# Optimization experiments

Measured on AMD Instinct MI355X. Metric: run time of the kernel, lower is better.

Reference implementation:

```python
import jax, jax.numpy as jnp
import numpy as np

# Module constants (from init_kwargs)
NUM_PREFIX = 8
NUM_LAYERS = 32
NUM_SUB = NUM_LAYERS - NUM_PREFIX  # 24
H = 32            # attention heads
RANK = 2          # scheduler_rank: heads are gated in groups of RANK
TAU = 5.0
HIDDEN = 4096
B = 16384


def setup_inputs() -> dict:
    key = jax.random.key(0)
    k1, k2, k3, k4 = jax.random.split(key, 4)
    x = jax.random.normal(k1, (B, HIDDEN), dtype=jnp.float32)
    latency = jax.random.uniform(k2, (B,), dtype=jnp.float32)
    W = jax.random.normal(k3, (HIDDEN, NUM_SUB * H * 2), dtype=jnp.float32) * 0.02
    b = jnp.zeros((NUM_SUB * H * 2,), dtype=jnp.float32)
    u = jax.random.uniform(k4, (B, NUM_SUB, H, 2), dtype=jnp.float32)
    return {"x": x, "latency": latency, "W": W, "b": b, "u": u}


def reference(x, latency, W, b, u):
    min_units = NUM_PREFIX * H // RANK   # 128
    max_units = NUM_LAYERS * H // RANK   # 512
    # latency_quantizing: snap continuous latency to integer head-group budget
    units = jnp.clip(jnp.round(latency * max_units), min_units, max_units)
    budget = units - min_units           # (B,) groups to activate in sub layers

    logits = (x @ W + b).reshape(B, NUM_SUB, H, 2)  # 2-way keep/drop per head

    # Gumbel-softmax (soft probs) from pre-sampled uniform noise
    eps = 1e-6
    g = -jnp.log(-jnp.log(u * (1.0 - 2.0 * eps) + eps))
    soft = jax.nn.softmax((logits + g) / TAU, axis=-1)  # (B, L, H, 2)
    p_keep = soft[..., 0]                               # (B, L, H)

    # Group heads by RANK, score groups, keep the top-`budget` groups per sample
    G = H // RANK
    scores = p_keep.reshape(B, NUM_SUB * G, RANK).mean(-1)   # (B, 384)
    ranks = jnp.argsort(jnp.argsort(-scores, axis=-1), axis=-1)
    hard_group = (ranks < budget[:, None]).astype(x.dtype)   # (B, 384)
    hard_keep = jnp.repeat(hard_group, RANK, axis=-1).reshape(B, NUM_SUB, H)
    hard = jnp.stack([hard_keep, 1.0 - hard_keep], axis=-1)  # (B, L, H, 2)

    # Straight-through hard sample
    out = hard + soft - jax.lax.stop_gradient(soft)          # (B, L, H, 2)
    out = jnp.moveaxis(out, -1, 2)                           # (B, L, 2, H)

    prefix = jnp.ones((B, NUM_PREFIX, 2, H), dtype=out.dtype)
    return jnp.concatenate([prefix, out], axis=1)            # (B, 32, 2, H)
```

## Files before the change

### kernel.cpp

```cpp
#include <hip/hip_runtime.h>
#include <math.h>

#define BATCH  16384
#define HID    4096
#define NCOLS  1536
#define NGRP   384

#define GAP_MIN 2.0e-5f
#define MARG    1.0e-5f
#define WMAX    16

typedef unsigned short u16;
typedef short bf16x8 __attribute__((ext_vector_type(8)));
typedef float f32x4  __attribute__((ext_vector_type(4)));

__device__ __forceinline__ int budget_of(float lat) {
    float un = rintf(lat * 512.0f);
    un = fminf(fmaxf(un, 128.0f), 512.0f);
    return (int)un - 128;
}

__device__ __forceinline__ double gumbel_d(float uu) {
    double v = (double)uu * (1.0 - 2.0e-6) + 1.0e-6;
    return -log(-log(v));
}

__device__ __forceinline__ float gumbel_f(float u) {
    float inner;
    if (u <= 0.5f) {
        float v = fmaf(u, 0.999998f, 1e-6f);
        inner = -logf(v);
    } else {
        float t1 = 1.0f - u;
        float w  = fmaf(1e-6f, fmaf(2.0f, u, -1.0f), t1);
        inner = -log1pf(-w);
    }
    return -logf(inner);
}

__device__ __forceinline__ float score_f(float l0, float l1, float l2, float l3,
                                         float4 uv) {
    const float d0 = ((l0 + gumbel_f(uv.x)) - (l1 + gumbel_f(uv.y))) * 0.2f;
    const float d1 = ((l2 + gumbel_f(uv.z)) - (l3 + gumbel_f(uv.w))) * 0.2f;
    const float p0 = 1.0f / (1.0f + expf(-d0));
    const float p1 = 1.0f / (1.0f + expf(-d1));
    return 0.5f * (p0 + p1);
}

__device__ __forceinline__ unsigned bf16_rne_bits(float f) {
    unsigned b = __float_as_uint(f);
    return (b + 0x7FFFu + ((b >> 16) & 1u)) >> 16;
}

__device__ __forceinline__ void split4(const float4 v, uint2& hi, uint2& lo) {
    const unsigned bx = __float_as_uint(v.x), by = __float_as_uint(v.y),
                   bz = __float_as_uint(v.z), bw = __float_as_uint(v.w);
    const unsigned hx = bx & 0xFFFF0000u, hy = by & 0xFFFF0000u,
                   hz = bz & 0xFFFF0000u, hw = bw & 0xFFFF0000u;
    hi.x = (hx >> 16) | hy;
    hi.y = (hz >> 16) | hw;
    const float lx = v.x - __uint_as_float(hx);
    const float ly = v.y - __uint_as_float(hy);
    const float lz = v.z - __uint_as_float(hz);
    const float lw = v.w - __uint_as_float(hw);
    lo.x = bf16_rne_bits(lx) | (bf16_rne_bits(ly) << 16);
    lo.y = bf16_rne_bits(lz) | (bf16_rne_bits(lw) << 16);
}

__device__ __forceinline__ void gload16(const u16* g, u16* l) {
    __builtin_amdgcn_global_load_lds(
        (const __attribute__((address_space(1))) unsigned int*)g,
        (__attribute__((address_space(3))) unsigned int*)l, 16, 0, 0);
}

__global__ __launch_bounds__(64)
void prefilter_kernel(const float* __restrict__ latency, float* __restrict__ out)
{
    const int b = blockIdx.x;
    const int t = threadIdx.x;
    const int budget = budget_of(latency[b]);
    float* obase = out + (size_t)b * 2048;

    const float4 ones = make_float4(1.f, 1.f, 1.f, 1.f);
    ((float4*)obase)[t]      = ones;
    ((float4*)obase)[t + 64] = ones;

    if (!(budget > 0 && budget < NGRP)) {
        const float K = (budget == 0) ? 0.0f : 1.0f;
#pragma unroll
        for (int j = 0; j < 6; ++j) {
            const int i = j * 64 + t;
            const int p = i * 4;
            const int s = (p >> 5) & 1;
            const float v = s ? (1.0f - K) : K;
            ((float4*)(obase + 512))[i] = make_float4(v, v, v, v);
        }
    }
}

__global__ __launch_bounds__(256)
void idx_build(const float* __restrict__ latency, int* __restrict__ count,
               int* __restrict__ idx)
{
    const int s = blockIdx.x * 256 + threadIdx.x;
    const int budget = budget_of(latency[s]);
    const bool interior = (budget > 0 && budget < NGRP);
    const unsigned long long m = __ballot(interior);
    const int lane = threadIdx.x & 63;
    int base = 0;
    if (lane == 0 && m) base = atomicAdd(count, __popcll(m));
    base = __shfl(base, 0);
    if (interior)
        idx[base + __popcll(m & ((1ull << lane) - 1ull))] = s;
}

__global__ __launch_bounds__(256)
void convert_w(const float* __restrict__ W, u16* __restrict__ wt_hi,
               u16* __restrict__ wt_lo)
{
    __shared__ float sT[32][33];
    const int n0 = blockIdx.x * 32, k0 = blockIdx.y * 32;
    const int t  = threadIdx.x;
    {
        const int lr = t >> 3, lc = (t & 7) * 4;
        const float4 v = *(const float4*)(W + (size_t)(k0 + lr) * NCOLS + n0 + lc);
        sT[lr][lc] = v.x; sT[lr][lc + 1] = v.y; sT[lr][lc + 2] = v.z; sT[lr][lc + 3] = v.w;
    }
    __syncthreads();
    const int ln = t >> 3, lk = (t & 7) * 4;
    unsigned hb[4], lb[4];
#pragma unroll
    for (int j = 0; j < 4; ++j) {
        const float xv = sT[lk + j][ln];
        const unsigned h = bf16_rne_bits(xv);
        const float hf = __uint_as_float(h << 16);
        hb[j] = h;
        lb[j] = bf16_rne_bits(xv - hf);
    }
    uint2 hw, lw;
    hw.x = hb[0] | (hb[1] << 16); hw.y = hb[2] | (hb[3] << 16);
    lw.x = lb[0] | (lb[1] << 16); lw.y = lb[2] | (lb[3] << 16);
    const int gn = n0 + ln;
    const size_t off = ((size_t)((gn >> 7) * 128 + (k0 >> 5)) * 4 + (lk >> 3)) * 1024
                     + (size_t)(gn & 127) * 8 + (lk & 7);
    *(uint2*)(wt_hi + off) = hw;
    *(uint2*)(wt_lo + off) = lw;
}

__global__ __launch_bounds__(256)
void gemm_bf16x3(const float* __restrict__ x, const u16* __restrict__ wt_hi,
                 const u16* __restrict__ wt_lo, const float* __restrict__ bias,
                 const float* __restrict__ uu, const int* __restrict__ idx,
                 const int* __restrict__ count, float* __restrict__ scoresf)
{
    __shared__ __align__(16) u16 sMem[2 * 5120 + 2 * 4096];
    __shared__ int rid[128];
    u16* const sAh = sMem;
    u16* const sAl = sMem + 5120;
    u16* const sBh = sMem + 10240;
    u16* const sBl = sMem + 14336;

    const int cnt  = *count;
    const int row0 = blockIdx.x * 128;
    if (row0 >= cnt) return;
    const int cb   = blockIdx.y;
    const int col0 = cb * 128;
    const int t    = threadIdx.x;

    if (t < 128) rid[t] = idx[min(row0 + t, cnt - 1)];
    __syncthreads();

    const int ar  = t >> 2;
    const int akc = (t & 3) << 3;
    const int arow  = ar * 40 + akc;
    const int arow2 = (ar + 64) * 40 + akc;
    const size_t xoff0 = (size_t)rid[ar] * HID + akc;
    const size_t xoff1 = (size_t)rid[ar + 64] * HID + akc;

    const int wave = t >> 6;
    const size_t bsrc0 = (size_t)cb * 524288 + (size_t)t * 8;
    const int ldsB0 = wave * 512;
    const int ldsB1 = 2048 + wave * 512;

    const int lane = t & 63;
    const int wr = wave >> 1;
    const int wc = wave & 1;
    const int fr = lane & 15;
    const int kb = lane >> 4;
    const int abase = (wr * 64 + fr) * 40 + kb * 8;
    const int bfrag = kb * 1024 + (wc * 64 + fr) * 8;

    f32x4 acc[4][4] = {};

    float4 a00 = *(const float4*)(x + xoff0);
    float4 a01 = *(const float4*)(x + xoff0 + 4);
    float4 a10 = *(const float4*)(x + xoff1);
    float4 a11 = *(const float4*)(x + xoff1 + 4);

#pragma unroll 1
    for (int k0 = 0; k0 < HID; k0 += 32) {
        __syncthreads();
        {
            uint2 h0, l0, h1, l1;
            split4(a00, h0, l0); split4(a01, h1, l1);
            *(uint4*)&sAh[arow]  = make_uint4(h0.x, h0.y, h1.x, h1.y);
            *(uint4*)&sAl[arow]  = make_uint4(l0.x, l0.y, l1.x, l1.y);
            split4(a10, h0, l0); split4(a11, h1, l1);
            *(uint4*)&sAh[arow2] = make_uint4(h0.x, h0.y, h1.x, h1.y);
            *(uint4*)&sAl[arow2] = make_uint4(l0.x, l0.y, l1.x, l1.y);
        }
        {
            const size_t bs = bsrc0 + (size_t)(k0 >> 5) * 4096;
            gload16(wt_hi + bs,        sBh + ldsB0);
            gload16(wt_hi + bs + 2048, sBh + ldsB1);
            gload16(wt_lo + bs,        sBl + ldsB0);
            gload16(wt_lo + bs + 2048, sBl + ldsB1);
        }
        __syncthreads();

        if (k0 + 32 < HID) {
            a00 = *(const float4*)(x + xoff0 + k0 + 32);
            a01 = *(const float4*)(x + xoff0 + k0 + 36);
            a10 = *(const float4*)(x + xoff1 + k0 + 32);
            a11 = *(const float4*)(x + xoff1 + k0 + 36);
        }

        bf16x8 bh[4], bl[4];
#pragma unroll
        for (int ni = 0; ni < 4; ++ni) {
            bh[ni] = *(const bf16x8*)&sBh[bfrag + ni * 128];
            bl[ni] = *(const bf16x8*)&sBl[bfrag + ni * 128];
        }
#pragma unroll
        for (int mi = 0; mi < 4; ++mi) {
            const bf16x8 ah = *(const bf16x8*)&sAh[abase + mi * 640];
            const bf16x8 al = *(const bf16x8*)&sAl[abase + mi * 640];
#pragma unroll
            for (int ni = 0; ni < 4; ++ni) {
                acc[mi][ni] = __builtin_amdgcn_mfma_f32_16x16x32_bf16(ah, bh[ni], acc[mi][ni], 0, 0, 0);
                acc[mi][ni] = __builtin_amdgcn_mfma_f32_16x16x32_bf16(ah, bl[ni], acc[mi][ni], 0, 0, 0);
                acc[mi][ni] = __builtin_amdgcn_mfma_f32_16x16x32_bf16(al, bh[ni], acc[mi][ni], 0, 0, 0);
            }
        }
    }

    float* const sOut = (float*)sMem;
    float* const sW   = sOut + wave * (16 * 68);
    const int gb = (col0 >> 2) + wc * 16;

#pragma unroll
    for (int mi = 0; mi < 4; ++mi) {
        __syncthreads();
#pragma unroll
        for (int ni = 0; ni < 4; ++ni)
#pragma unroll
            for (int r = 0; r < 4; ++r)
                sW[(kb * 4 + r) * 68 + ni * 16 + fr] = acc[mi][ni][r];
        __syncthreads();

        const int lr    = fr;
        const int gq    = kb;
        const int row_l = wr * 64 + mi * 16 + lr;
        const int cr    = row0 + row_l;
        const int orig  = rid[row_l];
        const float* so = sW + lr * 68 + gq * 16;
        const int g0    = gb + gq * 4;

        float s[4];
#pragma unroll
        for (int j = 0; j < 4; ++j) {
            const int g = g0 + j;
            const float4 lv = *(const float4*)(so + 4 * j);
            const float4 bv = *(const float4*)(bias + 4 * g);
            const float4 uv = *(const float4*)(uu + (size_t)orig * NCOLS + 4 * g);
            s[j] = score_f(lv.x + bv.x, lv.y + bv.y, lv.z + bv.z, lv.w + bv.w, uv);
        }
        *(float4*)&scoresf[(size_t)cr * NGRP + g0] = make_float4(s[0], s[1], s[2], s[3]);
    }
}

__global__ __launch_bounds__(384)
void select_fast(const float* __restrict__ scoresf, const float* __restrict__ latency,
                 const int* __restrict__ idx, const int* __restrict__ count,
                 float* __restrict__ out, int* __restrict__ ridx,
                 int* __restrict__ rcount, int* __restrict__ rcount2)
{
    const int b = blockIdx.x;
    if (b >= *count) return;
    const int t = threadIdx.x;
    const int orig = idx[b];

    __shared__ __align__(16) unsigned smu[NGRP];
    __shared__ float wred0[6], wred1[6];
    __shared__ int   flag;
    const float sg = scoresf[(size_t)b * NGRP + t];
    const unsigned bg = __float_as_uint(sg);
    smu[t] = bg;
    if (t == 0) flag = 0;
    const int budget = budget_of(latency[orig]);
    __syncthreads();

    int rank = 0;
#pragma unroll 4
    for (int j = 0; j < NGRP; j += 4) {
        const uint4 v = *(const uint4*)&smu[j];
        rank += (v.x > bg) ? 1 : 0;
        rank += (v.y > bg) ? 1 : 0;
        rank += (v.z > bg) ? 1 : 0;
        rank += (v.w > bg) ? 1 : 0;
    }
    const bool kept = (rank < budget);
    const int  ck   = __syncthreads_count(kept ? 1 : 0);

    if (ck != budget) {
        if (t == 0) { int s2 = atomicAdd(rcount2, 1); ridx[16383 - s2] = orig | (b << 14); }
        return;
    }

    float kv = kept ? sg : 3.0e38f;
    float dv = kept ? -3.0e38f : sg;
#pragma unroll
    for (int off = 32; off; off >>= 1) {
        kv = fminf(kv, __shfl_xor(kv, off));
        dv = fmaxf(dv, __shfl_xor(dv, off));
    }
    if ((t & 63) == 0) { wred0[t >> 6] = kv; wred1[t >> 6] = dv; }
    __syncthreads();
    if (t == 0) {
        float b0 = wred0[0], b1 = wred1[0];
#pragma unroll
        for (int w = 1; w < 6; ++w) { b0 = fminf(b0, wred0[w]); b1 = fmaxf(b1, wred1[w]); }
        if (b0 - b1 < GAP_MIN) { flag = 1; ridx[atomicAdd(rcount, 1)] = orig | (b << 14); }
    }
    __syncthreads();
    if (flag) return;

    const float keep = kept ? 1.0f : 0.0f;
    float* p = out + (size_t)orig * 2048 + 512 + (size_t)(t >> 4) * 64;
    const int h2 = (t & 15) << 1;
    *(float2*)(p + h2)      = make_float2(keep, keep);
    *(float2*)(p + 32 + h2) = make_float2(1.0f - keep, 1.0f - keep);
}

__global__ __launch_bounds__(384)
void window_repair(const float* __restrict__ x, const float* __restrict__ W,
                   const float* __restrict__ bias, const float* __restrict__ u,
                   const float* __restrict__ latency, const float* __restrict__ scoresf,
                   int* __restrict__ ridx, const int* __restrict__ rcount,
                   int* __restrict__ rcount2, float* __restrict__ out)
{
    __shared__ __align__(16) unsigned smu[NGRP];
    __shared__ float  wred0[6], wred1[6];
    __shared__ float  sbnd[2];
    __shared__ double red[6][4];
    __shared__ double s64[WMAX];
    __shared__ int    wg[WMAX];
    __shared__ int    wcnt;

    const int nrep = *rcount;
    const int t = threadIdx.x;

    for (int ib = blockIdx.x; ib < nrep; ib += gridDim.x) {
        const int pk   = ridx[ib];
        const int orig = pk & 0x3FFF;
        const int row  = pk >> 14;

        const float sg = scoresf[(size_t)row * NGRP + t];
        const unsigned bg = __float_as_uint(sg);
        smu[t] = bg;
        if (t == 0) wcnt = 0;
        const int budget = budget_of(latency[orig]);
        __syncthreads();

        int rank = 0;
#pragma unroll 4
        for (int j = 0; j < NGRP; j += 4) {
            const uint4 v = *(const uint4*)&smu[j];
            rank += (v.x > bg) ? 1 : 0;
            rank += (v.y > bg) ? 1 : 0;
            rank += (v.z > bg) ? 1 : 0;
            rank += (v.w > bg) ? 1 : 0;
        }
        const bool kept = (rank < budget);
        const int  ck   = __syncthreads_count(kept ? 1 : 0);

        if (ck != budget) {
            if (t == 0) { int s2 = atomicAdd(rcount2, 1); ridx[16383 - s2] = pk; }
            __syncthreads();
            continue;
        }
        float kv = kept ? sg : 3.0e38f;
        float dv = kept ? -3.0e38f : sg;
#pragma unroll
        for (int off = 32; off; off >>= 1) {
            kv = fminf(kv, __shfl_xor(kv, off));
            dv = fmaxf(dv, __shfl_xor(dv, off));
        }
        if ((t & 63) == 0) { wred0[t >> 6] = kv; wred1[t >> 6] = dv; }
        __syncthreads();
        if (t == 0) {
            float v0 = wred0[0], v1 = wred1[0];
#pragma unroll
            for (int w = 1; w < 6; ++w) { v0 = fminf(v0, wred0[w]); v1 = fmaxf(v1, wred1[w]); }
            sbnd[0] = v0; sbnd[1] = v1;
        }
        __syncthreads();

        const float b0 = sbnd[0], b1 = sbnd[1];
        const bool hi  = sg > b0 + MARG;
        const bool lo  = sg < b1 - MARG;
        int e_t = -1;
        if (!hi && !lo) {
            e_t = atomicAdd(&wcnt, 1);
            if (e_t < WMAX) wg[e_t] = t;
        }
        const int c_hi   = __syncthreads_count(hi ? 1 : 0);
        const int wcount = wcnt;

        if (wcount > WMAX) {
            if (t == 0) { int s2 = atomicAdd(rcount2, 1); ridx[16383 - s2] = pk; }
            __syncthreads();
            continue;
        }
        const int kwin = budget - c_hi;

        const float* xr = x + (size_t)orig * HID;
        for (int e = 0; e < wcount; ++e) {
            const int g = wg[e];
            double p0 = 0, p1 = 0, p2 = 0, p3 = 0;
            const float* wcp = W + 4 * g;
            for (int k = t; k < HID; k += 384) {
                const double xv = (double)xr[k];
                const float4 wv = *(const float4*)(wcp + (size_t)k * NCOLS);
                p0 = fma(xv, (double)wv.x, p0);
                p1 = fma(xv, (double)wv.y, p1);
                p2 = fma(xv, (double)wv.z, p2);
                p3 = fma(xv, (double)wv.w, p3);
            }
#pragma unroll
            for (int off = 32; off; off >>= 1) {
                p0 += __shfl_down(p0, off);
                p1 += __shfl_down(p1, off);
                p2 += __shfl_down(p2, off);
                p3 += __shfl_down(p3, off);
            }
            const int wid = t >> 6;
            if ((t & 63) == 0) {
                red[wid][0] = p0; red[wid][1] = p1;
                red[wid][2] = p2; red[wid][3] = p3;
            }
            __syncthreads();
            if (t == 0) {
                double l0 = (double)bias[4 * g + 0], l1 = (double)bias[4 * g + 1];
                double l2 = (double)bias[4 * g + 2], l3 = (double)bias[4 * g + 3];
                for (int w = 0; w < 6; ++w) {
                    l0 += red[w][0]; l1 += red[w][1];
                    l2 += red[w][2]; l3 += red[w][3];
                }
                const float4 uv = *(const float4*)(u + (size_t)orig * NCOLS + 4 * g);
                const double d0 = ((l0 + gumbel_d(uv.x)) - (l1 + gumbel_d(uv.y))) / 5.0;
                const double d1 = ((l2 + gumbel_d(uv.z)) - (l3 + gumbel_d(uv.w))) / 5.0;
                const double q0 = 1.0 / (1.0 + exp(-d0));
                const double q1 = 1.0 / (1.0 + exp(-d1));
                s64[e] = 0.5 * (q0 + q1);
            }
            __syncthreads();
        }

        float keep;
        if (hi)      keep = 1.0f;
        else if (lo) keep = 0.0f;
        else {
            const double se = s64[e_t];
            int r = 0;
            for (int f = 0; f < wcount; ++f)
                r += (s64[f] > se || (s64[f] == se && wg[f] < t)) ? 1 : 0;
            keep = (r < kwin) ? 1.0f : 0.0f;
        }
        float* pp = out + (size_t)orig * 2048 + 512 + (size_t)(t >> 4) * 64;
        const int h2 = (t & 15) << 1;
        *(float2*)(pp + h2)      = make_float2(keep, keep);
        *(float2*)(pp + 32 + h2) = make_float2(1.0f - keep, 1.0f - keep);
        __syncthreads();
    }
}

__global__ __launch_bounds__(256)
void gemm64_repair(const float* __restrict__ x, const float* __restrict__ W,
                   const float* __restrict__ bias, const float* __restrict__ u,
                   const int* __restrict__ ridx, const int* __restrict__ rcount2,
                   double* __restrict__ scores)
{
    __shared__ float As[16][36];
    __shared__ float Bs[16][68];
    __shared__ int   rid[32];

    const int cnt  = *rcount2;
    const int row0 = blockIdx.y * 32;
    if (row0 >= cnt) return;
    const int col0 = blockIdx.x * 64;
    const int t    = threadIdx.x;

    if (t < 32) rid[t] = ridx[16383 - min(row0 + t, cnt - 1)] & 0x3FFF;
    __syncthreads();

    const bool doA = (t < 128);
    const int ar  = t >> 2;
    const int akc = (t & 3) << 2;
    const int bkr = t >> 4;
    const int bnc = (t & 15) << 2;

    size_t xoff = 0;
    if (doA) xoff = (size_t)rid[ar] * HID + akc;
    const float* wp = W + (size_t)bkr * NCOLS + col0 + bnc;

    const int ty = t >> 4;
    const int tx = t & 15;

    double acc[2][4] = {};

    float4 a0 = make_float4(0, 0, 0, 0);
    if (doA) a0 = *(const float4*)(x + xoff);
    float4 b0 = *(const float4*)(wp);

    for (int k0 = 0; k0 < HID; k0 += 16) {
        __syncthreads();
        if (doA) {
            As[akc + 0][ar] = a0.x; As[akc + 1][ar] = a0.y;
            As[akc + 2][ar] = a0.z; As[akc + 3][ar] = a0.w;
        }
        *(float4*)&Bs[bkr][bnc] = b0;
        __syncthreads();
        if (k0 + 16 < HID) {
            if (doA) a0 = *(const float4*)(x + xoff + k0 + 16);
            b0 = *(const float4*)(wp + (size_t)(k0 + 16) * NCOLS);
        }
#pragma unroll
        for (int k = 0; k < 16; ++k) {
            const double a0d = (double)As[k][ty * 2];
            const double a1d = (double)As[k][ty * 2 + 1];
            const float4 bf  = *(const float4*)&Bs[k][tx * 4];
            const double bd[4] = {(double)bf.x, (double)bf.y, (double)bf.z, (double)bf.w};
#pragma unroll
            for (int j = 0; j < 4; ++j) {
                acc[0][j] = fma(a0d, bd[j], acc[0][j]);
                acc[1][j] = fma(a1d, bd[j], acc[1][j]);
            }
        }
    }

    const int g = (col0 >> 2) + tx;
    const double bs0 = (double)bias[4 * g + 0];
    const double bs1 = (double)bias[4 * g + 1];
    const double bs2 = (double)bias[4 * g + 2];
    const double bs3 = (double)bias[4 * g + 3];
#pragma unroll
    for (int i = 0; i < 2; ++i) {
        const int rl   = ty * 2 + i;
        const int cr   = row0 + rl;
        const int orig = rid[rl];
        const float4 uv = *(const float4*)(u + (size_t)orig * NCOLS + 4 * g);
        const double l0 = acc[i][0] + bs0;
        const double l1 = acc[i][1] + bs1;
        const double l2 = acc[i][2] + bs2;
        const double l3 = acc[i][3] + bs3;
        const double d0 = ((l0 + gumbel_d(uv.x)) - (l1 + gumbel_d(uv.y))) / 5.0;
        const double d1 = ((l2 + gumbel_d(uv.z)) - (l3 + gumbel_d(uv.w))) / 5.0;
        const double p0 = 1.0 / (1.0 + exp(-d0));
        const double p1 = 1.0 / (1.0 + exp(-d1));
        scores[(size_t)cr * NGRP + g] = 0.5 * (p0 + p1);
    }
}

__global__ __launch_bounds__(384)
void select_repair(const double* __restrict__ scores, const float* __restrict__ latency,
                   const int* __restrict__ ridx, const int* __restrict__ rcount2,
                   float* __restrict__ out)
{
    const int b = blockIdx.x;
    if (b >= *rcount2) return;
    const int t = threadIdx.x;
    const int orig = ridx[16383 - b] & 0x3FFF;

    __shared__ __align__(16) double sm[NGRP];
    const double sg = scores[(size_t)b * NGRP + t];
    sm[t] = sg;
    const int budget = budget_of(latency[orig]);
    __syncthreads();

    int rank = 0;
#pragma unroll 4
    for (int j = 0; j < NGRP; j += 2) {
        const double2 v = *(const double2*)&sm[j];
        rank += (v.x > sg || (v.x == sg && (j + 0) < t)) ? 1 : 0;
        rank += (v.y > sg || (v.y == sg && (j + 1) < t)) ? 1 : 0;
    }
    const float keep = (rank < budget) ? 1.0f : 0.0f;

    float* p = out + (size_t)orig * 2048 + 512 + (size_t)(t >> 4) * 64;
    const int h2 = (t & 15) << 1;
    *(float2*)(p + h2)      = make_float2(keep, keep);
    *(float2*)(p + 32 + h2) = make_float2(1.0f - keep, 1.0f - keep);
}

extern "C" void kernel_launch(void* const* d_in, const int* in_sizes, int n_in,
                              void* d_out, int out_size, void* d_ws, size_t ws_size,
                              hipStream_t stream) {
    const float* x       = (const float*)d_in[0];
    const float* latency = (const float*)d_in[1];
    const float* W       = (const float*)d_in[2];
    const float* bias    = (const float*)d_in[3];
    const float* u       = (const float*)d_in[4];
    float* out           = (float*)d_out;

    int*    count   = (int*)d_ws;
    int*    rcount  = (int*)((char*)d_ws + 4);
    int*    rcount2 = (int*)((char*)d_ws + 8);
    int*    idx     = (int*)((char*)d_ws + 256);
    int*    ridx    = (int*)((char*)d_ws + 256 + 65536);
    u16*    wt_hi   = (u16*)((char*)d_ws + 131328);
    u16*    wt_lo   = (u16*)((char*)d_ws + 131328 + 12582912);
    float*  scoresf = (float*)((char*)d_ws + 131328 + 25165824);
    double* scores64= (double*)((char*)d_ws + 131328);

    hipMemsetAsync(d_ws, 0, 256, stream);
    convert_w<<<dim3(NCOLS / 32, HID / 32), 256, 0, stream>>>(W, wt_hi, wt_lo);
    prefilter_kernel<<<BATCH, 64, 0, stream>>>(latency, out);
    idx_build<<<BATCH / 256, 256, 0, stream>>>(latency, count, idx);
    gemm_bf16x3<<<dim3(BATCH / 128, NCOLS / 128), 256, 0, stream>>>(
        x, wt_hi, wt_lo, bias, u, idx, count, scoresf);
    select_fast<<<BATCH, NGRP, 0, stream>>>(scoresf, latency, idx, count, out,
                                            ridx, rcount, rcount2);
    window_repair<<<1024, NGRP, 0, stream>>>(x, W, bias, u, latency, scoresf,
                                             ridx, rcount, rcount2, out);
    gemm64_repair<<<dim3(NCOLS / 64, BATCH / 32), 256, 0, stream>>>(
        x, W, bias, u, ridx, rcount2, scores64);
    select_repair<<<BATCH, NGRP, 0, stream>>>(scores64, latency, ridx, rcount2, out);
}
```

Before: 1.093 ms.

## Replace O(n²) rank counting with radix-select threshold and shrink repair grids

The fast selection kernel now finds the budget-th largest score with a byte-wise radix select (a histogram per byte via wave ballots plus a prefix scan), instead of having every thread compare against all 384 scores. Ties at the threshold are routed to the repair path. The repair GEMM and repair select kernels become grid-stride loops over small fixed grids, so far fewer empty blocks are launched, and the prefilter packs four samples per block. The radix select adds several block syncs and LDS atomics per sample, which could cost as much as the simple compare loop it replaces.

```diff
diff --git a/kernel.cpp b/kernel.cpp
--- a/kernel.cpp
+++ b/kernel.cpp
@@ -73,23 +73,23 @@
         (__attribute__((address_space(3))) unsigned int*)l, 16, 0, 0);
 }
 
-__global__ __launch_bounds__(64)
+__global__ __launch_bounds__(256)
 void prefilter_kernel(const float* __restrict__ latency, float* __restrict__ out)
 {
-    const int b = blockIdx.x;
-    const int t = threadIdx.x;
+    const int b = blockIdx.x * 4 + (threadIdx.x >> 6);
+    const int lane = threadIdx.x & 63;
     const int budget = budget_of(latency[b]);
     float* obase = out + (size_t)b * 2048;
 
     const float4 ones = make_float4(1.f, 1.f, 1.f, 1.f);
-    ((float4*)obase)[t]      = ones;
-    ((float4*)obase)[t + 64] = ones;
+    ((float4*)obase)[lane]      = ones;
+    ((float4*)obase)[lane + 64] = ones;
 
     if (!(budget > 0 && budget < NGRP)) {
         const float K = (budget == 0) ? 0.0f : 1.0f;
 #pragma unroll
         for (int j = 0; j < 6; ++j) {
-            const int i = j * 64 + t;
+            const int i = j * 64 + lane;
             const int p = i * 4;
             const int s = (p >> 5) & 1;
             const float v = s ? (1.0f - K) : K;
@@ -290,47 +290,85 @@
     const int t = threadIdx.x;
     const int orig = idx[b];
 
-    __shared__ __align__(16) unsigned smu[NGRP];
-    __shared__ float wred0[6], wred1[6];
+    __shared__ int   hist[4][256];
+    __shared__ int   wtot[4];
+    __shared__ int   sel[3];
+    __shared__ float wred1[6];
     __shared__ int   flag;
+
     const float sg = scoresf[(size_t)b * NGRP + t];
     const unsigned bg = __float_as_uint(sg);
-    smu[t] = bg;
+    const int budget = budget_of(latency[orig]);
+    const int lane = t & 63;
+
+    for (int i = t; i < 1024; i += 384) (&hist[0][0])[i] = 0;
     if (t == 0) flag = 0;
-    const int budget = budget_of(latency[orig]);
     __syncthreads();
 
-    int rank = 0;
-#pragma unroll 4
-    for (int j = 0; j < NGRP; j += 4) {
-        const uint4 v = *(const uint4*)&smu[j];
-        rank += (v.x > bg) ? 1 : 0;
-        rank += (v.y > bg) ? 1 : 0;
-        rank += (v.z > bg) ? 1 : 0;
-        rank += (v.w > bg) ? 1 : 0;
-    }
-    const bool kept = (rank < budget);
-    const int  ck   = __syncthreads_count(kept ? 1 : 0);
-
-    if (ck != budget) {
+    unsigned prefix = 0;
+    int r = budget, ceq = 0;
+
+#pragma unroll
+    for (int p = 3; p >= 0; --p) {
+        const int shift = 8 * p;
+        const bool match = (p == 3) ? true : (((bg ^ prefix) >> (shift + 8)) == 0);
+        const unsigned byte = (bg >> shift) & 255u;
+        unsigned long long same = __ballot(match);
+#pragma unroll
+        for (int bit = 0; bit < 8; ++bit) {
+            const unsigned long long bb = __ballot((byte >> bit) & 1u);
+            same &= ((byte >> bit) & 1u) ? bb : ~bb;
+        }
+        if (match && (same & ((1ull << lane) - 1ull)) == 0)
+            atomicAdd(&hist[p][byte], (int)__popcll(same));
+        __syncthreads();
+
+        int v = 0, incl = 0;
+        if (t < 256) {
+            v = hist[p][t];
+            incl = v;
+#pragma unroll
+            for (int off = 1; off < 64; off <<= 1) {
+                const int pv = __shfl(incl, (lane + off) & 63);
+                incl += (lane + off < 64) ? pv : 0;
+            }
+            if (lane == 0) wtot[t >> 6] = incl;
+        }
+        __syncthreads();
+        if (t < 256) {
+            const int w = t >> 6;
+            int add = 0;
+            if (w < 1) add += wtot[1];
+            if (w < 2) add += wtot[2];
+            if (w < 3) add += wtot[3];
+            const int S_incl = incl + add;
+            const int S_excl = S_incl - v;
+            if (S_excl < r && r <= S_incl) { sel[0] = t; sel[1] = S_excl; sel[2] = v; }
+        }
+        __syncthreads();
+        prefix |= ((unsigned)sel[0]) << shift;
+        r   -= sel[1];
+        ceq  = sel[2];
+    }
+
+    if (r < ceq) {
         if (t == 0) { int s2 = atomicAdd(rcount2, 1); ridx[16383 - s2] = orig | (b << 14); }
         return;
     }
-
-    float kv = kept ? sg : 3.0e38f;
+    const bool kept = (bg >= prefix);
+
     float dv = kept ? -3.0e38f : sg;
 #pragma unroll
-    for (int off = 32; off; off >>= 1) {
-        kv = fminf(kv, __shfl_xor(kv, off));
-        dv = fmaxf(dv, __shfl_xor(dv, off));
-    }
-    if ((t & 63) == 0) { wred0[t >> 6] = kv; wred1[t >> 6] = dv; }
+    for (int off = 32; off; off >>= 1) dv = fmaxf(dv, __shfl_xor(dv, off));
+    if (lane == 0) wred1[t >> 6] = dv;
     __syncthreads();
     if (t == 0) {
-        float b0 = wred0[0], b1 = wred1[0];
-#pragma unroll
-        for (int w = 1; w < 6; ++w) { b0 = fminf(b0, wred0[w]); b1 = fmaxf(b1, wred1[w]); }
-        if (b0 - b1 < GAP_MIN) { flag = 1; ridx[atomicAdd(rcount, 1)] = orig | (b << 14); }
+        float b1 = wred1[0];
+#pragma unroll
+        for (int w = 1; w < 6; ++w) b1 = fmaxf(b1, wred1[w]);
+        if (__uint_as_float(prefix) - b1 < GAP_MIN) {
+            flag = 1; ridx[atomicAdd(rcount, 1)] = orig | (b << 14);
+        }
     }
     __syncthreads();
     if (flag) return;
@@ -496,79 +534,80 @@
     __shared__ int   rid[32];
 
     const int cnt  = *rcount2;
-    const int row0 = blockIdx.y * 32;
-    if (row0 >= cnt) return;
     const int col0 = blockIdx.x * 64;
     const int t    = threadIdx.x;
 
-    if (t < 32) rid[t] = ridx[16383 - min(row0 + t, cnt - 1)] & 0x3FFF;
-    __syncthreads();
-
-    const bool doA = (t < 128);
-    const int ar  = t >> 2;
-    const int akc = (t & 3) << 2;
-    const int bkr = t >> 4;
-    const int bnc = (t & 15) << 2;
-
-    size_t xoff = 0;
-    if (doA) xoff = (size_t)rid[ar] * HID + akc;
-    const float* wp = W + (size_t)bkr * NCOLS + col0 + bnc;
-
-    const int ty = t >> 4;
-    const int tx = t & 15;
-
-    double acc[2][4] = {};
-
-    float4 a0 = make_float4(0, 0, 0, 0);
-    if (doA) a0 = *(const float4*)(x + xoff);
-    float4 b0 = *(const float4*)(wp);
-
-    for (int k0 = 0; k0 < HID; k0 += 16) {
-        __syncthreads();
-        if (doA) {
-            As[akc + 0][ar] = a0.x; As[akc + 1][ar] = a0.y;
-            As[akc + 2][ar] = a0.z; As[akc + 3][ar] = a0.w;
-        }
-        *(float4*)&Bs[bkr][bnc] = b0;
-        __syncthreads();
-        if (k0 + 16 < HID) {
-            if (doA) a0 = *(const float4*)(x + xoff + k0 + 16);
-            b0 = *(const float4*)(wp + (size_t)(k0 + 16) * NCOLS);
-        }
-#pragma unroll
-        for (int k = 0; k < 16; ++k) {
-            const double a0d = (double)As[k][ty * 2];
-            const double a1d = (double)As[k][ty * 2 + 1];
-            const float4 bf  = *(const float4*)&Bs[k][tx * 4];
-            const double bd[4] = {(double)bf.x, (double)bf.y, (double)bf.z, (double)bf.w};
-#pragma unroll
-            for (int j = 0; j < 4; ++j) {
-                acc[0][j] = fma(a0d, bd[j], acc[0][j]);
-                acc[1][j] = fma(a1d, bd[j], acc[1][j]);
-            }
-        }
-    }
-
-    const int g = (col0 >> 2) + tx;
-    const double bs0 = (double)bias[4 * g + 0];
-    const double bs1 = (double)bias[4 * g + 1];
-    const double bs2 = (double)bias[4 * g + 2];
-    const double bs3 = (double)bias[4 * g + 3];
-#pragma unroll
-    for (int i = 0; i < 2; ++i) {
-        const int rl   = ty * 2 + i;
-        const int cr   = row0 + rl;
-        const int orig = rid[rl];
-        const float4 uv = *(const float4*)(u + (size_t)orig * NCOLS + 4 * g);
-        const double l0 = acc[i][0] + bs0;
-        const double l1 = acc[i][1] + bs1;
-        const double l2 = acc[i][2] + bs2;
-        const double l3 = acc[i][3] + bs3;
-        const double d0 = ((l0 + gumbel_d(uv.x)) - (l1 + gumbel_d(uv.y))) / 5.0;
-        const double d1 = ((l2 + gumbel_d(uv.z)) - (l3 + gumbel_d(uv.w))) / 5.0;
-        const double p0 = 1.0 / (1.0 + exp(-d0));
-        const double p1 = 1.0 / (1.0 + exp(-d1));
-        scores[(size_t)cr * NGRP + g] = 0.5 * (p0 + p1);
+    for (int row0 = blockIdx.y * 32; row0 < cnt; row0 += gridDim.y * 32) {
+        if (t < 32) rid[t] = ridx[16383 - min(row0 + t, cnt - 1)] & 0x3FFF;
+        __syncthreads();
+
+        const bool doA = (t < 128);
+        const int ar  = t >> 2;
+        const int akc = (t & 3) << 2;
+        const int bkr = t >> 4;
+        const int bnc = (t & 15) << 2;
+
+        size_t xoff = 0;
+        if (doA) xoff = (size_t)rid[ar] * HID + akc;
+        const float* wp = W + (size_t)bkr * NCOLS + col0 + bnc;
+
+        const int ty = t >> 4;
+        const int tx = t & 15;
+
+        double acc[2][4] = {};
+
+        float4 a0 = make_float4(0, 0, 0, 0);
+        if (doA) a0 = *(const float4*)(x + xoff);
+        float4 b0 = *(const float4*)(wp);
+
+        for (int k0 = 0; k0 < HID; k0 += 16) {
+            __syncthreads();
+            if (doA) {
+                As[akc + 0][ar] = a0.x; As[akc + 1][ar] = a0.y;
+                As[akc + 2][ar] = a0.z; As[akc + 3][ar] = a0.w;
+            }
+            *(float4*)&Bs[bkr][bnc] = b0;
+            __syncthreads();
+            if (k0 + 16 < HID) {
+                if (doA) a0 = *(const float4*)(x + xoff + k0 + 16);
+                b0 = *(const float4*)(wp + (size_t)(k0 + 16) * NCOLS);
+            }
+#pragma unroll
+            for (int k = 0; k < 16; ++k) {
+                const double a0d = (double)As[k][ty * 2];
+                const double a1d = (double)As[k][ty * 2 + 1];
+                const float4 bf  = *(const float4*)&Bs[k][tx * 4];
+                const double bd[4] = {(double)bf.x, (double)bf.y, (double)bf.z, (double)bf.w};
+#pragma unroll
+                for (int j = 0; j < 4; ++j) {
+                    acc[0][j] = fma(a0d, bd[j], acc[0][j]);
+                    acc[1][j] = fma(a1d, bd[j], acc[1][j]);
+                }
+            }
+        }
+
+        const int g = (col0 >> 2) + tx;
+        const double bs0 = (double)bias[4 * g + 0];
+        const double bs1 = (double)bias[4 * g + 1];
+        const double bs2 = (double)bias[4 * g + 2];
+        const double bs3 = (double)bias[4 * g + 3];
+#pragma unroll
+        for (int i = 0; i < 2; ++i) {
+            const int rl   = ty * 2 + i;
+            const int cr   = row0 + rl;
+            const int orig = rid[rl];
+            const float4 uv = *(const float4*)(u + (size_t)orig * NCOLS + 4 * g);
+            const double l0 = acc[i][0] + bs0;
+            const double l1 = acc[i][1] + bs1;
+            const double l2 = acc[i][2] + bs2;
+            const double l3 = acc[i][3] + bs3;
+            const double d0 = ((l0 + gumbel_d(uv.x)) - (l1 + gumbel_d(uv.y))) / 5.0;
+            const double d1 = ((l2 + gumbel_d(uv.z)) - (l3 + gumbel_d(uv.w))) / 5.0;
+            const double p0 = 1.0 / (1.0 + exp(-d0));
+            const double p1 = 1.0 / (1.0 + exp(-d1));
+            scores[(size_t)cr * NGRP + g] = 0.5 * (p0 + p1);
+        }
+        __syncthreads();
     }
 }
 
@@ -577,30 +616,33 @@
                    const int* __restrict__ ridx, const int* __restrict__ rcount2,
                    float* __restrict__ out)
 {
-    const int b = blockIdx.x;
-    if (b >= *rcount2) return;
+    const int cnt = *rcount2;
     const int t = threadIdx.x;
-    const int orig = ridx[16383 - b] & 0x3FFF;
-
     __shared__ __align__(16) double sm[NGRP];
-    const double sg = scores[(size_t)b * NGRP + t];
-    sm[t] = sg;
-    const int budget = budget_of(latency[orig]);
-    __syncthreads();
-
-    int rank = 0;
+
+    for (int b = blockIdx.x; b < cnt; b += gridDim.x) {
+        const int orig = ridx[16383 - b] & 0x3FFF;
+
+        const double sg = scores[(size_t)b * NGRP + t];
+        sm[t] = sg;
+        const int budget = budget_of(latency[orig]);
+        __syncthreads();
+
+        int rank = 0;
 #pragma unroll 4
-    for (int j = 0; j < NGRP; j += 2) {
-        const double2 v = *(const double2*)&sm[j];
-        rank += (v.x > sg || (v.x == sg && (j + 0) < t)) ? 1 : 0;
-        rank += (v.y > sg || (v.y == sg && (j + 1) < t)) ? 1 : 0;
-    }
-    const float keep = (rank < budget) ? 1.0f : 0.0f;
-
-    float* p = out + (size_t)orig * 2048 + 512 + (size_t)(t >> 4) * 64;
-    const int h2 = (t & 15) << 1;
-    *(float2*)(p + h2)      = make_float2(keep, keep);
-    *(float2*)(p + 32 + h2) = make_float2(1.0f - keep, 1.0f - keep);
+        for (int j = 0; j < NGRP; j += 2) {
+            const double2 v = *(const double2*)&sm[j];
+            rank += (v.x > sg || (v.x == sg && (j + 0) < t)) ? 1 : 0;
+            rank += (v.y > sg || (v.y == sg && (j + 1) < t)) ? 1 : 0;
+        }
+        const float keep = (rank < budget) ? 1.0f : 0.0f;
+
+        float* p = out + (size_t)orig * 2048 + 512 + (size_t)(t >> 4) * 64;
+        const int h2 = (t & 15) << 1;
+        *(float2*)(p + h2)      = make_float2(keep, keep);
+        *(float2*)(p + 32 + h2) = make_float2(1.0f - keep, 1.0f - keep);
+        __syncthreads();
+    }
 }
 
 extern "C" void kernel_launch(void* const* d_in, const int* in_sizes, int n_in,
@@ -625,7 +667,7 @@
 
     hipMemsetAsync(d_ws, 0, 256, stream);
     convert_w<<<dim3(NCOLS / 32, HID / 32), 256, 0, stream>>>(W, wt_hi, wt_lo);
-    prefilter_kernel<<<BATCH, 64, 0, stream>>>(latency, out);
+    prefilter_kernel<<<BATCH / 4, 256, 0, stream>>>(latency, out);
     idx_build<<<BATCH / 256, 256, 0, stream>>>(latency, count, idx);
     gemm_bf16x3<<<dim3(BATCH / 128, NCOLS / 128), 256, 0, stream>>>(
         x, wt_hi, wt_lo, bias, u, idx, count, scoresf);
@@ -633,7 +675,7 @@
                                             ridx, rcount, rcount2);
     window_repair<<<1024, NGRP, 0, stream>>>(x, W, bias, u, latency, scoresf,
                                              ridx, rcount, rcount2, out);
-    gemm64_repair<<<dim3(NCOLS / 64, BATCH / 32), 256, 0, stream>>>(
+    gemm64_repair<<<dim3(NCOLS / 64, 16), 256, 0, stream>>>(
         x, W, bias, u, ridx, rcount2, scores64);
-    select_repair<<<BATCH, NGRP, 0, stream>>>(scores64, latency, ridx, rcount2, out);
-}
+    select_repair<<<512, NGRP, 0, stream>>>(scores64, latency, ridx, rcount2, out);
+}
```

New measurement: 1.043 ms. 1.05x faster.
